# Performance work log

Hardware: AMD Instinct MI355X
Metric: run time of the kernel (lower is better)

Reference implementation:

```python
import jax, jax.numpy as jnp
import numpy as np

B, S, H = 16, 8192, 256

def setup_inputs() -> dict:
    key = jax.random.key(0)
    k1, k2, k3, k4, k5 = jax.random.split(key, 5)
    scale = 1.0 / np.sqrt(H)
    return {
        "hidden": jax.random.normal(k1, (B, H), dtype=jnp.float32),
        "encoder_outputs": jax.random.normal(k2, (B, S, H), dtype=jnp.float32),
        "W1": jax.random.uniform(k3, (H, H), dtype=jnp.float32, minval=-scale, maxval=scale),
        "W2": jax.random.uniform(k4, (H, H), dtype=jnp.float32, minval=-scale, maxval=scale),
        "V": jax.random.uniform(k5, (1, H), dtype=jnp.float32, minval=-scale, maxval=scale),
    }

def reference(hidden, encoder_outputs, W1, W2, V):
    # hidden: [B, H], encoder_outputs: [B, S, H]
    h1 = jnp.einsum('bh,kh->bk', hidden, W1)[:, None, :]        # [B, 1, H]
    h2 = jnp.einsum('bsh,kh->bsk', encoder_outputs, W2)          # [B, S, H]
    scores = jnp.einsum('bsh,oh->bso', jnp.tanh(h1 + h2), V)     # [B, S, 1]
    attn = jax.nn.softmax(scores, axis=1)                        # softmax over seq dim
    context = jnp.sum(attn * encoder_outputs, axis=1)            # [B, H]
    # torch: unsqueeze/transpose/repeat/squeeze/permute -> tile context over seq: [B, H, S]
    context_tiled = jnp.broadcast_to(context[:, :, None], (context.shape[0], context.shape[1], encoder_outputs.shape[1]))
    return (context_tiled, context, attn[:, :, 0])
```

## Files before the change

### kernel.cpp

```cpp
#include <hip/hip_runtime.h>
#include <hip/hip_bf16.h>
#include <math.h>

#define B_ 16
#define S_ 8192
#define H_ 256
#define NBLK 32
#define TILE_R 32
#define T_PER_BLK 8
#define LROW 264

using bf16x8 = __attribute__((ext_vector_type(8))) short;
using f32x4 = __attribute__((ext_vector_type(4))) float;

__device__ inline short f2bf(float x) {
  union {
    float f;
    unsigned u;
  } v;
  v.f = x;
  unsigned r = v.u + 0x7FFFu + ((v.u >> 16) & 1u);
  return (short)(r >> 16);
}

__device__ inline bf16x8 pack8(float4 a, float4 b) {
  union {
    __hip_bfloat162 h[4];
    bf16x8 v;
  } u;
  u.h[0] = __float22bfloat162_rn(make_float2(a.x, a.y));
  u.h[1] = __float22bfloat162_rn(make_float2(a.z, a.w));
  u.h[2] = __float22bfloat162_rn(make_float2(b.x, b.y));
  u.h[3] = __float22bfloat162_rn(make_float2(b.z, b.w));
  return u.v;
}

__device__ inline float fast_tanh(float x) {
  float e = exp2f(x * 2.885390082f);
  return fmaf(-2.f, __builtin_amdgcn_rcpf(e + 1.f), 1.f);
}

__global__ __launch_bounds__(256) void prep_kernel(
    const float* __restrict__ hidden, const float* __restrict__ W1,
    const float* __restrict__ W2, short* __restrict__ W2f,
    float* __restrict__ h1) {
  const int blk = blockIdx.x;
  const int t = threadIdx.x;
  if (blk < 32) {
    const int gid = blk * 256 + t;
    const int l = gid & 63;
    const int j0 = (gid >> 6) & 15;
    const int ks = gid >> 10;
    const int row = j0 * 16 + (l & 15);
    const int col = ks * 32 + (l >> 4) * 8;
    const float* wp = W2 + row * H_ + col;
    bf16x8 out;
#pragma unroll
    for (int i = 0; i < 8; ++i) out[i] = f2bf(wp[i]);
    *(bf16x8*)(W2f + (size_t)gid * 8) = out;
  } else {
    const int b = blk - 32;
    const float* hrow = hidden + b * H_;
    const float* wrow = W1 + t * H_;
    float acc = 0.f;
#pragma unroll 8
    for (int h = 0; h < H_; ++h) acc += hrow[h] * wrow[h];
    h1[b * H_ + t] = acc;
  }
}

__global__ __launch_bounds__(512, 4) void scores_ctx_kernel(
    const float* __restrict__ enc, const short* __restrict__ W2f,
    const float* __restrict__ h1, const float* __restrict__ V,
    float* __restrict__ expsc, float* __restrict__ c_blk,
    float* __restrict__ l_blk) {
  __shared__ __align__(16) short albuf[2][TILE_R * LROW];
  __shared__ float pcomb[8][33];
  __shared__ float avec[TILE_R];
  __shared__ float2 clds2[4][129];
  __shared__ float lsum[8];

  const int tid = threadIdx.x;
  const int w = tid >> 6;
  const int l = tid & 63;
  const int lo = l & 15;
  const int hi = l >> 4;
  const int bid = blockIdx.x;
  const int b = bid >> 5;
  const int blk = bid & 31;
  const int s_base = blk * (TILE_R * T_PER_BLK);

  const bf16x8* bbase = (const bf16x8*)W2f;
  bf16x8 bfrag[8][2];
#pragma unroll
  for (int ks = 0; ks < 8; ++ks)
#pragma unroll
    for (int jj = 0; jj < 2; ++jj)
      bfrag[ks][jj] = bbase[(ks * 16 + (2 * w + jj)) * 64 + l];

  float h1v[2], Vv[2];
#pragma unroll
  for (int jj = 0; jj < 2; ++jj) {
    h1v[jj] = h1[b * H_ + (2 * w + jj) * 16 + lo];
    Vv[jj] = V[(2 * w + jj) * 16 + lo];
  }

  const int r0 = tid >> 5;
  const int kc0 = tid & 31;
  const float4* gsrc = (const float4*)(enc + (size_t)b * S_ * H_);
  const int gbase = r0 * 64 + kc0 * 2;

  const int rg = tid >> 7;
  const int cp = tid & 127;
  float c0 = 0.f, c1 = 0.f, l_part = 0.f;

  {
    const int gi0 = s_base * 64 + gbase;
    const int gi1 = gi0 + 16 * 64;
    float4 a0 = gsrc[gi0], a1 = gsrc[gi0 + 1];
    float4 b0 = gsrc[gi1], b1 = gsrc[gi1 + 1];
    *(bf16x8*)&albuf[0][r0 * LROW + kc0 * 8] = pack8(a0, a1);
    *(bf16x8*)&albuf[0][(r0 + 16) * LROW + kc0 * 8] = pack8(b0, b1);
  }
  __syncthreads();

  const int b0s = lo & 1;
  const int b1s = (lo >> 1) & 1;
  const int b2s = (lo >> 2) & 1;

  for (int t = 0; t < T_PER_BLK; ++t) {
    const int cur = t & 1;

    f32x4 acc[2][2];
#pragma unroll
    for (int m = 0; m < 2; ++m)
#pragma unroll
      for (int jj = 0; jj < 2; ++jj) acc[m][jj] = (f32x4){0.f, 0.f, 0.f, 0.f};

    const short* abase = &albuf[cur][lo * LROW + hi * 8];
#pragma unroll
    for (int ks = 0; ks < 8; ++ks) {
      bf16x8 a0 = *(const bf16x8*)(abase + ks * 32);
      bf16x8 a1 = *(const bf16x8*)(abase + 16 * LROW + ks * 32);
      acc[0][0] = __builtin_amdgcn_mfma_f32_16x16x32_bf16(a0, bfrag[ks][0], acc[0][0], 0, 0, 0);
      acc[0][1] = __builtin_amdgcn_mfma_f32_16x16x32_bf16(a0, bfrag[ks][1], acc[0][1], 0, 0, 0);
      acc[1][0] = __builtin_amdgcn_mfma_f32_16x16x32_bf16(a1, bfrag[ks][0], acc[1][0], 0, 0, 0);
      acc[1][1] = __builtin_amdgcn_mfma_f32_16x16x32_bf16(a1, bfrag[ks][1], acc[1][1], 0, 0, 0);
    }

    float4 na0, na1, nb0, nb1;
    if (t + 1 < T_PER_BLK) {
      const int gi0 = (s_base + (t + 1) * TILE_R) * 64 + gbase;
      const int gi1 = gi0 + 16 * 64;
      na0 = gsrc[gi0];
      na1 = gsrc[gi0 + 1];
      nb0 = gsrc[gi1];
      nb1 = gsrc[gi1 + 1];
    }

    float p0 = fast_tanh(acc[0][0][0] + h1v[0]) * Vv[0] + fast_tanh(acc[0][1][0] + h1v[1]) * Vv[1];
    float p1 = fast_tanh(acc[0][0][1] + h1v[0]) * Vv[0] + fast_tanh(acc[0][1][1] + h1v[1]) * Vv[1];
    float p2 = fast_tanh(acc[0][0][2] + h1v[0]) * Vv[0] + fast_tanh(acc[0][1][2] + h1v[1]) * Vv[1];
    float p3 = fast_tanh(acc[0][0][3] + h1v[0]) * Vv[0] + fast_tanh(acc[0][1][3] + h1v[1]) * Vv[1];
    float p4 = fast_tanh(acc[1][0][0] + h1v[0]) * Vv[0] + fast_tanh(acc[1][1][0] + h1v[1]) * Vv[1];
    float p5 = fast_tanh(acc[1][0][1] + h1v[0]) * Vv[0] + fast_tanh(acc[1][1][1] + h1v[1]) * Vv[1];
    float p6 = fast_tanh(acc[1][0][2] + h1v[0]) * Vv[0] + fast_tanh(acc[1][1][2] + h1v[1]) * Vv[1];
    float p7 = fast_tanh(acc[1][0][3] + h1v[0]) * Vv[0] + fast_tanh(acc[1][1][3] + h1v[1]) * Vv[1];

    float q0 = (b0s ? p1 : p0) + __shfl_xor((b0s ? p0 : p1), 1, 16);
    float q1 = (b0s ? p3 : p2) + __shfl_xor((b0s ? p2 : p3), 1, 16);
    float q2 = (b0s ? p5 : p4) + __shfl_xor((b0s ? p4 : p5), 1, 16);
    float q3 = (b0s ? p7 : p6) + __shfl_xor((b0s ? p6 : p7), 1, 16);
    float r0q = (b1s ? q1 : q0) + __shfl_xor((b1s ? q0 : q1), 2, 16);
    float r1q = (b1s ? q3 : q2) + __shfl_xor((b1s ? q2 : q3), 2, 16);
    float u = (b2s ? r1q : r0q) + __shfl_xor((b2s ? r0q : r1q), 4, 16);
    u += __shfl_xor(u, 8, 16);

    if (lo < 8) {
      const int row = ((lo >> 2) & 1) * 16 + hi * 4 + (lo & 3);
      pcomb[w][row] = u;
    }
    __syncthreads();

    if (t + 1 < T_PER_BLK) {
      *(bf16x8*)&albuf[cur ^ 1][r0 * LROW + kc0 * 8] = pack8(na0, na1);
      *(bf16x8*)&albuf[cur ^ 1][(r0 + 16) * LROW + kc0 * 8] = pack8(nb0, nb1);
    }

    if (l < 4) {
      const int row = w * 4 + l;
      float s = 0.f;
#pragma unroll
      for (int ww = 0; ww < 8; ++ww) s += pcomb[ww][row];
      float e = exp2f(s * 1.44269504f);
      avec[row] = e;
      expsc[(size_t)b * S_ + s_base + t * TILE_R + row] = e;
      l_part += e;
    }
    __syncthreads();

    const unsigned* ab32 = (const unsigned*)&albuf[cur][0];
#pragma unroll
    for (int k = 0; k < 8; ++k) {
      const int r = rg * 8 + k;
      unsigned vb = ab32[r * 132 + cp];
      float a = avec[r];
      float he = __uint_as_float(vb << 16);
      float ho = __uint_as_float(vb & 0xFFFF0000u);
      c0 = fmaf(a, he, c0);
      c1 = fmaf(a, ho, c1);
    }
  }

  float lp = l_part;
  lp += __shfl_xor(lp, 1);
  lp += __shfl_xor(lp, 2);
  if (l == 0) lsum[w] = lp;
  clds2[rg][cp] = make_float2(c0, c1);
  __syncthreads();
  if (tid < 128) {
    float2 s0 = clds2[0][tid], s1 = clds2[1][tid];
    float2 s2 = clds2[2][tid], s3 = clds2[3][tid];
    float2 r;
    r.x = s0.x + s1.x + s2.x + s3.x;
    r.y = s0.y + s1.y + s2.y + s3.y;
    ((float2*)(c_blk + ((size_t)(b * NBLK + blk)) * H_))[tid] = r;
  }
  if (tid == 0) {
    float ls = 0.f;
#pragma unroll
    for (int ww = 0; ww < 8; ++ww) ls += lsum[ww];
    l_blk[b * NBLK + blk] = ls;
  }
}

__global__ __launch_bounds__(256) void finish_kernel(
    const float* __restrict__ expsc, const float* __restrict__ l_blk,
    const float* __restrict__ c_blk, float* __restrict__ out0,
    float* __restrict__ out1, float* __restrict__ out2) {
  const int bx = blockIdx.x;
  const int b = blockIdx.y;
  const int tid = threadIdx.x;
  float lg = 0.f;
#pragma unroll
  for (int j = 0; j < NBLK; ++j) lg += l_blk[b * NBLK + j];
  const float inv = 1.f / lg;

  if (bx < 4) {
    const size_t base = (size_t)b * S_ + bx * 2048;
    const float4* ip = (const float4*)(expsc + base);
    float4* op = (float4*)(out2 + base);
    float4 x0 = ip[tid * 2];
    float4 x1 = ip[tid * 2 + 1];
    float4 y0 = {x0.x * inv, x0.y * inv, x0.z * inv, x0.w * inv};
    float4 y1 = {x1.x * inv, x1.y * inv, x1.z * inv, x1.w * inv};
    op[tid * 2] = y0;
    op[tid * 2 + 1] = y1;
  } else {
    const int h = bx - 4;
    float cs = 0.f;
#pragma unroll
    for (int j = 0; j < NBLK; ++j)
      cs += c_blk[((size_t)(b * NBLK + j)) * H_ + h];
    const float ctx = cs * inv;
    if (tid == 0) out1[b * H_ + h] = ctx;
    float4 vv = {ctx, ctx, ctx, ctx};
    float4* op = (float4*)(out0 + ((size_t)b * H_ + h) * S_);
#pragma unroll 4
    for (int i = tid; i < S_ / 4; i += 256) op[i] = vv;
  }
}

extern "C" void kernel_launch(void* const* d_in, const int* in_sizes, int n_in,
                              void* d_out, int out_size, void* d_ws,
                              size_t ws_size, hipStream_t stream) {
  const float* hidden = (const float*)d_in[0];
  const float* enc = (const float*)d_in[1];
  const float* W1 = (const float*)d_in[2];
  const float* W2 = (const float*)d_in[3];
  const float* V = (const float*)d_in[4];

  float* out0 = (float*)d_out;
  float* out1 = out0 + (size_t)B_ * H_ * S_;
  float* out2 = out1 + B_ * H_;

  float* ws = (float*)d_ws;
  short* W2f = (short*)ws;
  float* h1 = ws + 32768;
  float* expsc = h1 + B_ * H_;
  float* l_blk = expsc + (size_t)B_ * S_;
  float* c_blk = l_blk + B_ * NBLK;

  prep_kernel<<<48, 256, 0, stream>>>(hidden, W1, W2, W2f, h1);
  scores_ctx_kernel<<<B_ * NBLK, 512, 0, stream>>>(enc, W2f, h1, V, expsc,
                                                   c_blk, l_blk);
  finish_kernel<<<dim3(H_ + 4, B_), 256, 0, stream>>>(expsc, l_blk, c_blk,
                                                      out0, out1, out2);
}
```

Baseline: 75.10 us.

## Process 64-row phases to halve block barriers and split prefetch across phase halves

Each loop iteration now covers 64 sequence rows instead of 32, done as two 32-row MFMA sub-tiles, so there are half as many iterations and __syncthreads pairs per block. The prefetch of the next phase is split into two halves issued at different points so global load latency overlaps the epilogue and the softmax/exp step. Shared memory doubles for the A buffer, which can lower occupancy, and each thread holds more registers in flight.

```diff
diff --git a/kernel.cpp b/kernel.cpp
--- a/kernel.cpp
+++ b/kernel.cpp
@@ -6,8 +6,8 @@
 #define S_ 8192
 #define H_ 256
 #define NBLK 32
-#define TILE_R 32
-#define T_PER_BLK 8
+#define PHASE_R 64
+#define P_PER_BLK 4
 #define LROW 264
 
 using bf16x8 = __attribute__((ext_vector_type(8))) short;
@@ -74,9 +74,9 @@
     const float* __restrict__ h1, const float* __restrict__ V,
     float* __restrict__ expsc, float* __restrict__ c_blk,
     float* __restrict__ l_blk) {
-  __shared__ __align__(16) short albuf[2][TILE_R * LROW];
-  __shared__ float pcomb[8][33];
-  __shared__ float avec[TILE_R];
+  __shared__ __align__(16) short albuf[2][PHASE_R * LROW];
+  __shared__ float pcomb[8][PHASE_R + 1];
+  __shared__ float avec[PHASE_R];
   __shared__ float2 clds2[4][129];
   __shared__ float lsum[8];
 
@@ -88,7 +88,7 @@
   const int bid = blockIdx.x;
   const int b = bid >> 5;
   const int blk = bid & 31;
-  const int s_base = blk * (TILE_R * T_PER_BLK);
+  const int s_base = blk * (PHASE_R * P_PER_BLK);
 
   const bf16x8* bbase = (const bf16x8*)W2f;
   bf16x8 bfrag[8][2];
@@ -115,12 +115,13 @@
   float c0 = 0.f, c1 = 0.f, l_part = 0.f;
 
   {
-    const int gi0 = s_base * 64 + gbase;
-    const int gi1 = gi0 + 16 * 64;
-    float4 a0 = gsrc[gi0], a1 = gsrc[gi0 + 1];
-    float4 b0 = gsrc[gi1], b1 = gsrc[gi1 + 1];
-    *(bf16x8*)&albuf[0][r0 * LROW + kc0 * 8] = pack8(a0, a1);
-    *(bf16x8*)&albuf[0][(r0 + 16) * LROW + kc0 * 8] = pack8(b0, b1);
+    const int gi = s_base * 64 + gbase;
+#pragma unroll
+    for (int g = 0; g < 4; ++g) {
+      float4 x0 = gsrc[gi + g * 16 * 64];
+      float4 x1 = gsrc[gi + g * 16 * 64 + 1];
+      *(bf16x8*)&albuf[0][(r0 + g * 16) * LROW + kc0 * 8] = pack8(x0, x1);
+    }
   }
   __syncthreads();
 
@@ -128,16 +129,47 @@
   const int b1s = (lo >> 1) & 1;
   const int b2s = (lo >> 2) & 1;
 
-  for (int t = 0; t < T_PER_BLK; ++t) {
+  for (int t = 0; t < P_PER_BLK; ++t) {
     const int cur = t & 1;
+    const short* abase = &albuf[cur][lo * LROW + hi * 8];
+
+#define EPILOGUE(roff)                                                        \
+  {                                                                           \
+    float p0 = fast_tanh(acc[0][0][0] + h1v[0]) * Vv[0] +                     \
+               fast_tanh(acc[0][1][0] + h1v[1]) * Vv[1];                      \
+    float p1 = fast_tanh(acc[0][0][1] + h1v[0]) * Vv[0] +                     \
+               fast_tanh(acc[0][1][1] + h1v[1]) * Vv[1];                      \
+    float p2 = fast_tanh(acc[0][0][2] + h1v[0]) * Vv[0] +                     \
+               fast_tanh(acc[0][1][2] + h1v[1]) * Vv[1];                      \
+    float p3 = fast_tanh(acc[0][0][3] + h1v[0]) * Vv[0] +                     \
+               fast_tanh(acc[0][1][3] + h1v[1]) * Vv[1];                      \
+    float p4 = fast_tanh(acc[1][0][0] + h1v[0]) * Vv[0] +                     \
+               fast_tanh(acc[1][1][0] + h1v[1]) * Vv[1];                      \
+    float p5 = fast_tanh(acc[1][0][1] + h1v[0]) * Vv[0] +                     \
+               fast_tanh(acc[1][1][1] + h1v[1]) * Vv[1];                      \
+    float p6 = fast_tanh(acc[1][0][2] + h1v[0]) * Vv[0] +                     \
+               fast_tanh(acc[1][1][2] + h1v[1]) * Vv[1];                      \
+    float p7 = fast_tanh(acc[1][0][3] + h1v[0]) * Vv[0] +                     \
+               fast_tanh(acc[1][1][3] + h1v[1]) * Vv[1];                      \
+    float q0 = (b0s ? p1 : p0) + __shfl_xor((b0s ? p0 : p1), 1, 16);          \
+    float q1 = (b0s ? p3 : p2) + __shfl_xor((b0s ? p2 : p3), 1, 16);          \
+    float q2 = (b0s ? p5 : p4) + __shfl_xor((b0s ? p4 : p5), 1, 16);          \
+    float q3 = (b0s ? p7 : p6) + __shfl_xor((b0s ? p6 : p7), 1, 16);          \
+    float r0q = (b1s ? q1 : q0) + __shfl_xor((b1s ? q0 : q1), 2, 16);         \
+    float r1q = (b1s ? q3 : q2) + __shfl_xor((b1s ? q2 : q3), 2, 16);         \
+    float u = (b2s ? r1q : r0q) + __shfl_xor((b2s ? r0q : r1q), 4, 16);       \
+    u += __shfl_xor(u, 8, 16);                                                \
+    if (lo < 8) {                                                             \
+      const int row = (roff) + ((lo >> 2) & 1) * 16 + hi * 4 + (lo & 3);      \
+      pcomb[w][row] = u;                                                      \
+    }                                                                         \
+  }
 
     f32x4 acc[2][2];
 #pragma unroll
     for (int m = 0; m < 2; ++m)
 #pragma unroll
       for (int jj = 0; jj < 2; ++jj) acc[m][jj] = (f32x4){0.f, 0.f, 0.f, 0.f};
-
-    const short* abase = &albuf[cur][lo * LROW + hi * 8];
 #pragma unroll
     for (int ks = 0; ks < 8; ++ks) {
       bf16x8 a0 = *(const bf16x8*)(abase + ks * 32);
@@ -147,62 +179,70 @@
       acc[1][0] = __builtin_amdgcn_mfma_f32_16x16x32_bf16(a1, bfrag[ks][0], acc[1][0], 0, 0, 0);
       acc[1][1] = __builtin_amdgcn_mfma_f32_16x16x32_bf16(a1, bfrag[ks][1], acc[1][1], 0, 0, 0);
     }
-
-    float4 na0, na1, nb0, nb1;
-    if (t + 1 < T_PER_BLK) {
-      const int gi0 = (s_base + (t + 1) * TILE_R) * 64 + gbase;
-      const int gi1 = gi0 + 16 * 64;
-      na0 = gsrc[gi0];
-      na1 = gsrc[gi0 + 1];
-      nb0 = gsrc[gi1];
-      nb1 = gsrc[gi1 + 1];
-    }
-
-    float p0 = fast_tanh(acc[0][0][0] + h1v[0]) * Vv[0] + fast_tanh(acc[0][1][0] + h1v[1]) * Vv[1];
-    float p1 = fast_tanh(acc[0][0][1] + h1v[0]) * Vv[0] + fast_tanh(acc[0][1][1] + h1v[1]) * Vv[1];
-    float p2 = fast_tanh(acc[0][0][2] + h1v[0]) * Vv[0] + fast_tanh(acc[0][1][2] + h1v[1]) * Vv[1];
-    float p3 = fast_tanh(acc[0][0][3] + h1v[0]) * Vv[0] + fast_tanh(acc[0][1][3] + h1v[1]) * Vv[1];
-    float p4 = fast_tanh(acc[1][0][0] + h1v[0]) * Vv[0] + fast_tanh(acc[1][1][0] + h1v[1]) * Vv[1];
-    float p5 = fast_tanh(acc[1][0][1] + h1v[0]) * Vv[0] + fast_tanh(acc[1][1][1] + h1v[1]) * Vv[1];
-    float p6 = fast_tanh(acc[1][0][2] + h1v[0]) * Vv[0] + fast_tanh(acc[1][1][2] + h1v[1]) * Vv[1];
-    float p7 = fast_tanh(acc[1][0][3] + h1v[0]) * Vv[0] + fast_tanh(acc[1][1][3] + h1v[1]) * Vv[1];
-
-    float q0 = (b0s ? p1 : p0) + __shfl_xor((b0s ? p0 : p1), 1, 16);
-    float q1 = (b0s ? p3 : p2) + __shfl_xor((b0s ? p2 : p3), 1, 16);
-    float q2 = (b0s ? p5 : p4) + __shfl_xor((b0s ? p4 : p5), 1, 16);
-    float q3 = (b0s ? p7 : p6) + __shfl_xor((b0s ? p6 : p7), 1, 16);
-    float r0q = (b1s ? q1 : q0) + __shfl_xor((b1s ? q0 : q1), 2, 16);
-    float r1q = (b1s ? q3 : q2) + __shfl_xor((b1s ? q2 : q3), 2, 16);
-    float u = (b2s ? r1q : r0q) + __shfl_xor((b2s ? r0q : r1q), 4, 16);
-    u += __shfl_xor(u, 8, 16);
-
-    if (lo < 8) {
-      const int row = ((lo >> 2) & 1) * 16 + hi * 4 + (lo & 3);
-      pcomb[w][row] = u;
-    }
+    EPILOGUE(0)
+
+#pragma unroll
+    for (int m = 0; m < 2; ++m)
+#pragma unroll
+      for (int jj = 0; jj < 2; ++jj) acc[m][jj] = (f32x4){0.f, 0.f, 0.f, 0.f};
+#pragma unroll
+    for (int ks = 0; ks < 8; ++ks) {
+      bf16x8 a0 = *(const bf16x8*)(abase + 32 * LROW + ks * 32);
+      bf16x8 a1 = *(const bf16x8*)(abase + 48 * LROW + ks * 32);
+      acc[0][0] = __builtin_amdgcn_mfma_f32_16x16x32_bf16(a0, bfrag[ks][0], acc[0][0], 0, 0, 0);
+      acc[0][1] = __builtin_amdgcn_mfma_f32_16x16x32_bf16(a0, bfrag[ks][1], acc[0][1], 0, 0, 0);
+      acc[1][0] = __builtin_amdgcn_mfma_f32_16x16x32_bf16(a1, bfrag[ks][0], acc[1][0], 0, 0, 0);
+      acc[1][1] = __builtin_amdgcn_mfma_f32_16x16x32_bf16(a1, bfrag[ks][1], acc[1][1], 0, 0, 0);
+    }
+
+    float4 a0A, a1A, b0A, b1A;
+    if (t + 1 < P_PER_BLK) {
+      const int gi = (s_base + (t + 1) * PHASE_R) * 64 + gbase;
+      a0A = gsrc[gi];
+      a1A = gsrc[gi + 1];
+      b0A = gsrc[gi + 16 * 64];
+      b1A = gsrc[gi + 16 * 64 + 1];
+    }
+
+    EPILOGUE(32)
+#undef EPILOGUE
+
     __syncthreads();
 
-    if (t + 1 < T_PER_BLK) {
-      *(bf16x8*)&albuf[cur ^ 1][r0 * LROW + kc0 * 8] = pack8(na0, na1);
-      *(bf16x8*)&albuf[cur ^ 1][(r0 + 16) * LROW + kc0 * 8] = pack8(nb0, nb1);
-    }
-
-    if (l < 4) {
-      const int row = w * 4 + l;
+    if (t + 1 < P_PER_BLK) {
+      *(bf16x8*)&albuf[cur ^ 1][r0 * LROW + kc0 * 8] = pack8(a0A, a1A);
+      *(bf16x8*)&albuf[cur ^ 1][(r0 + 16) * LROW + kc0 * 8] = pack8(b0A, b1A);
+    }
+    float4 a0B, a1B, b0B, b1B;
+    if (t + 1 < P_PER_BLK) {
+      const int gi = (s_base + (t + 1) * PHASE_R + 32) * 64 + gbase;
+      a0B = gsrc[gi];
+      a1B = gsrc[gi + 1];
+      b0B = gsrc[gi + 16 * 64];
+      b1B = gsrc[gi + 16 * 64 + 1];
+    }
+
+    if (l < 8) {
+      const int row = w * 8 + l;
       float s = 0.f;
 #pragma unroll
       for (int ww = 0; ww < 8; ++ww) s += pcomb[ww][row];
       float e = exp2f(s * 1.44269504f);
       avec[row] = e;
-      expsc[(size_t)b * S_ + s_base + t * TILE_R + row] = e;
+      expsc[(size_t)b * S_ + s_base + t * PHASE_R + row] = e;
       l_part += e;
     }
+
+    if (t + 1 < P_PER_BLK) {
+      *(bf16x8*)&albuf[cur ^ 1][(r0 + 32) * LROW + kc0 * 8] = pack8(a0B, a1B);
+      *(bf16x8*)&albuf[cur ^ 1][(r0 + 48) * LROW + kc0 * 8] = pack8(b0B, b1B);
+    }
     __syncthreads();
 
     const unsigned* ab32 = (const unsigned*)&albuf[cur][0];
 #pragma unroll
-    for (int k = 0; k < 8; ++k) {
-      const int r = rg * 8 + k;
+    for (int k = 0; k < 16; ++k) {
+      const int r = rg * 16 + k;
       unsigned vb = ab32[r * 132 + cp];
       float a = avec[r];
       float he = __uint_as_float(vb << 16);
@@ -215,6 +255,7 @@
   float lp = l_part;
   lp += __shfl_xor(lp, 1);
   lp += __shfl_xor(lp, 2);
+  lp += __shfl_xor(lp, 4);
   if (l == 0) lsum[w] = lp;
   clds2[rg][cp] = make_float2(c0, c1);
   __syncthreads();
```

New measurement: 79.26 us. 5.5% more time.
